# Optimization experiments

Hardware: AMD Instinct MI355X
Metric: run time of the kernel (lower is better)

## Reference

```python
import jax, jax.numpy as jnp
import numpy as np

NUM_CLASSES = 101
BATCH = 262144
LAMBDA = 1000.0


def setup_inputs() -> dict:
    key = jax.random.key(0)
    k1, k2 = jax.random.split(key)
    outputs = jax.random.normal(k1, (BATCH, NUM_CLASSES), dtype=jnp.float32)
    targets = jax.random.randint(k2, (BATCH,), 0, NUM_CLASSES, dtype=jnp.int64)
    return {"outputs": outputs, "targets": targets}


def reference(outputs, targets):
    B, C = outputs.shape
    targets = targets.reshape(-1)
    tf = targets.astype(outputs.dtype)

    probs = jax.nn.softmax(outputs, axis=1)                      # [B, C]
    labels = jnp.arange(C, dtype=outputs.dtype)                  # [C]
    pred_values = jnp.sum(probs * labels[None, :], axis=1)       # [B]
    centered = labels[None, :] - pred_values[:, None]            # [B, C]
    variance = jnp.sum(probs * centered * centered, axis=1)      # [B]
    variance = jnp.clip(variance, 1e-6, None)
    est_err = (pred_values - tf) ** 2
    concentrated_loss = jnp.mean(0.5 * jnp.log(variance) + est_err / (2.0 * variance))

    # Unimodal ordinal penalty, vectorized over the original double loop:
    # sign_j = -1 if j < target else +1; penalty = relu(-(p_j - p_{j+1}) * sign_j)
    j = jnp.arange(C - 1)                                        # [C-1]
    sign = jnp.where(j[None, :] < targets[:, None], -1.0, 1.0).astype(outputs.dtype)
    prob_diff = probs[:, :-1] - probs[:, 1:]                     # [B, C-1]
    penalty = jax.nn.relu(-prob_diff * sign)
    unimodal_loss = jnp.sum(penalty) / B
    weighted_unimodal_loss = LAMBDA * unimodal_loss

    total_loss = concentrated_loss + weighted_unimodal_loss
    return (total_loss, concentrated_loss, weighted_unimodal_loss)
```

## Files before the change

kernel.cpp:

```cpp
#include <hip/hip_runtime.h>


#define NT 128
#define TR 128
#define NC 101
#define TILE_F4 3232
#define PAD_F4 3328
#define NBLK 512
#define LAMBDA_W 1000.0

__device__ __forceinline__ void gload_lds16(const float4* g, float4* l)
{
    __builtin_amdgcn_global_load_lds(
        (const __attribute__((address_space(1))) void*)g,
        (__attribute__((address_space(3))) void*)l,
        16, 0, 0);
}

__device__ __forceinline__ void prefetch_tile(const float4* __restrict__ g4,
                                              float4* l4, int tid)
{
#pragma unroll
    for (int k = 0; k < 25; ++k)
        gload_lds16(g4 + k * NT + tid, l4 + k * NT + tid);
    if (tid < 32)
        gload_lds16(g4 + 25 * NT + tid, l4 + 25 * NT + tid);
}

__global__ __launch_bounds__(NT)
void ucl_row_kernel(const float* __restrict__ x,
                    const int* __restrict__ tgt,
                    float2* __restrict__ partial,
                    int ntiles)
{
    __shared__ __align__(16) float4 buf[2][PAD_F4];
    __shared__ float red[4];

    const int tid = threadIdx.x;
    const int bid = blockIdx.x;
    const int nb  = gridDim.x;

    const int tpb   = ntiles / nb;
    const int rem   = ntiles - tpb * nb;
    const int start = bid * tpb + (bid < rem ? bid : rem);
    const int cnt   = tpb + (bid < rem ? 1 : 0);

    const float4* __restrict__ x4 = (const float4*)x;

    int t_cur = tgt[(size_t)start * TR + tid];
    prefetch_tile(x4 + (size_t)start * TILE_F4, buf[0], tid);

    float conc = 0.f, pens = 0.f;

    for (int i = 0; i < cnt; ++i) {
        __syncthreads();

        if (i + 1 < cnt)
            prefetch_tile(x4 + (size_t)(start + i + 1) * TILE_F4,
                          buf[(i + 1) & 1], tid);
        int t_next = (i + 1 < cnt) ? tgt[(size_t)(start + i + 1) * TR + tid] : 0;

        const float* __restrict__ xr = (const float*)buf[i & 1] + tid * NC;
        const int t = t_cur;

        float e = __expf(xr[0]);
        float S = e, W = 0.f, Q = 0.f, pen = 0.f, ep = e;
#pragma unroll
        for (int j = 1; j < NC; ++j) {
            float e2 = __expf(xr[j]);
            float fj = (float)j;
            S += e2;
            W = fmaf(e2, fj, W);
            Q = fmaf(e2, fj * fj, Q);
            float d = ep - e2;
            float r = ((j - 1) < t) ? d : -d;
            pen += fmaxf(r, 0.f);
            ep = e2;
        }
        float pred = W / S;
        float var  = fmaxf(fmaf(-pred, pred, Q / S), 1e-6f);
        float err  = pred - (float)t;
        conc += 0.5f * __logf(var) + err * err / (2.0f * var);
        pens += pen / S;

        t_cur = t_next;
    }

#pragma unroll
    for (int off = 32; off > 0; off >>= 1) {
        conc += __shfl_down(conc, off);
        pens += __shfl_down(pens, off);
    }
    if ((tid & 63) == 0) {
        red[(tid >> 6) * 2 + 0] = conc;
        red[(tid >> 6) * 2 + 1] = pens;
    }
    __syncthreads();
    if (tid == 0)
        partial[bid] = make_float2(red[0] + red[2], red[1] + red[3]);
}

__global__ __launch_bounds__(256)
void ucl_finalize(const float2* __restrict__ partial,
                  float* __restrict__ out,
                  int nblocks, double invB)
{
    const int tid = threadIdx.x;
    double c = 0.0, p = 0.0;
    for (int i = tid; i < nblocks; i += 256) {
        float2 v = partial[i];
        c += (double)v.x;
        p += (double)v.y;
    }
#pragma unroll
    for (int off = 32; off > 0; off >>= 1) {
        c += __shfl_down(c, off);
        p += __shfl_down(p, off);
    }
    __shared__ double s[8];
    if ((tid & 63) == 0) { s[(tid >> 6) * 2] = c; s[(tid >> 6) * 2 + 1] = p; }
    __syncthreads();
    if (tid == 0) {
        double C = (s[0] + s[2] + s[4] + s[6]) * invB;
        double P = (s[1] + s[3] + s[5] + s[7]) * invB * LAMBDA_W;
        out[0] = (float)(C + P);
        out[1] = (float)C;
        out[2] = (float)P;
    }
}

extern "C" void kernel_launch(void* const* d_in, const int* in_sizes, int n_in,
                              void* d_out, int out_size, void* d_ws, size_t ws_size,
                              hipStream_t stream)
{
    const float* x   = (const float*)d_in[0];
    const int*   tgt = (const int*)d_in[1];
    float* out = (float*)d_out;
    float2* partial = (float2*)d_ws;

    const int B = in_sizes[1];
    const int ntiles = B / TR;
    const int blocks = (ntiles < NBLK) ? ntiles : NBLK;

    hipLaunchKernelGGL(ucl_row_kernel, dim3(blocks), dim3(NT), 0, stream,
                       x, tgt, partial, ntiles);
    hipLaunchKernelGGL(ucl_finalize, dim3(1), dim3(256), 0, stream,
                       partial, out, blocks, 1.0 / (double)B);
}
```

Measured before the change: 173.9 us.

## Split each row across four threads and launch one block per tile

Replaces the persistent double-buffered 512-block kernel with one 512-thread block per 128-row tile. Each row's 101 classes are split into four quarter scans, with one thread per quarter, and the partial sums are combined through LDS. The unimodal penalty is rewritten algebraically as a sum of positive diffs plus a boundary term minus the target probability. The aim is more waves in flight and a shorter serial exp chain per thread. In exchange it drops the cross-tile prefetch overlap and adds extra barriers and a per-block partial, with 2048 partials for the finalize to reduce.

```diff
diff --git a/kernel.cpp b/kernel.cpp
--- a/kernel.cpp
+++ b/kernel.cpp
@@ -1,12 +1,10 @@
 #include <hip/hip_runtime.h>
 
 
-#define NT 128
+#define NT 512
 #define TR 128
 #define NC 101
 #define TILE_F4 3232
-#define PAD_F4 3328
-#define NBLK 512
 #define LAMBDA_W 1000.0
 
 __device__ __forceinline__ void gload_lds16(const float4* g, float4* l)
@@ -17,73 +15,88 @@
         16, 0, 0);
 }
 
-__device__ __forceinline__ void prefetch_tile(const float4* __restrict__ g4,
-                                              float4* l4, int tid)
+template<int LO, int HI>
+__device__ __forceinline__ void scan_quarter(const float* __restrict__ xr, int t,
+                                             float& S, float& W, float& Q, float& pen)
 {
+    float e = __expf(xr[LO]);
+    S = e;
+    W = (float)LO * e;
+    Q = (float)(LO * LO) * e;
+    pen = 0.f;
+    float ep = e;
 #pragma unroll
-    for (int k = 0; k < 25; ++k)
-        gload_lds16(g4 + k * NT + tid, l4 + k * NT + tid);
-    if (tid < 32)
-        gload_lds16(g4 + 25 * NT + tid, l4 + 25 * NT + tid);
+    for (int j = LO + 1; j < HI; ++j) {
+        float e2 = __expf(xr[j]);
+        S += e2;
+        W = fmaf(e2, (float)j, W);
+        Q = fmaf(e2, (float)(j * j), Q);
+        pen += fmaxf(ep - e2, 0.f);
+        ep = e2;
+    }
+    if (HI < NC) {
+        float e2 = __expf(xr[HI]);
+        pen += fmaxf(ep - e2, 0.f);
+    } else {
+        pen += ep;
+    }
+    if (t >= LO && t < HI)
+        pen -= __expf(xr[t]);
 }
 
-__global__ __launch_bounds__(NT)
+__global__ __launch_bounds__(NT, 6)
 void ucl_row_kernel(const float* __restrict__ x,
                     const int* __restrict__ tgt,
-                    float2* __restrict__ partial,
-                    int ntiles)
+                    float2* __restrict__ partial)
 {
-    __shared__ __align__(16) float4 buf[2][PAD_F4];
+    __shared__ __align__(16) float tile[TR * NC];
     __shared__ float red[4];
 
     const int tid = threadIdx.x;
     const int bid = blockIdx.x;
-    const int nb  = gridDim.x;
+    const int r   = tid & (TR - 1);
+    const int q   = tid >> 7;
 
-    const int tpb   = ntiles / nb;
-    const int rem   = ntiles - tpb * nb;
-    const int start = bid * tpb + (bid < rem ? bid : rem);
-    const int cnt   = tpb + (bid < rem ? 1 : 0);
+    {
+        const float4* __restrict__ g4 =
+            (const float4*)(x + (size_t)bid * (TR * NC));
+        float4* l4 = (float4*)tile;
+#pragma unroll
+        for (int k = 0; k < 6; ++k)
+            gload_lds16(g4 + k * NT + tid, l4 + k * NT + tid);
+        if (tid < TILE_F4 - 6 * NT)
+            gload_lds16(g4 + 6 * NT + tid, l4 + 6 * NT + tid);
+    }
+    const int t = tgt[(size_t)bid * TR + r];
+    __syncthreads();
 
-    const float4* __restrict__ x4 = (const float4*)x;
+    const float* __restrict__ xr = tile + r * NC;
+    float S, W, Q, pen;
+    if      (q == 0) scan_quarter< 0,  26>(xr, t, S, W, Q, pen);
+    else if (q == 1) scan_quarter<26,  51>(xr, t, S, W, Q, pen);
+    else if (q == 2) scan_quarter<51,  76>(xr, t, S, W, Q, pen);
+    else             scan_quarter<76, 101>(xr, t, S, W, Q, pen);
 
-    int t_cur = tgt[(size_t)start * TR + tid];
-    prefetch_tile(x4 + (size_t)start * TILE_F4, buf[0], tid);
+    __syncthreads();
+    {
+        float4* p4 = (float4*)(tile + r * 20 + q * 4);
+        *p4 = make_float4(S, W, Q, pen);
+    }
+    __syncthreads();
 
     float conc = 0.f, pens = 0.f;
-
-    for (int i = 0; i < cnt; ++i) {
-        __syncthreads();
-
-        if (i + 1 < cnt)
-            prefetch_tile(x4 + (size_t)(start + i + 1) * TILE_F4,
-                          buf[(i + 1) & 1], tid);
-        int t_next = (i + 1 < cnt) ? tgt[(size_t)(start + i + 1) * TR + tid] : 0;
-
-        const float* __restrict__ xr = (const float*)buf[i & 1] + tid * NC;
-        const int t = t_cur;
-
-        float e = __expf(xr[0]);
-        float S = e, W = 0.f, Q = 0.f, pen = 0.f, ep = e;
-#pragma unroll
-        for (int j = 1; j < NC; ++j) {
-            float e2 = __expf(xr[j]);
-            float fj = (float)j;
-            S += e2;
-            W = fmaf(e2, fj, W);
-            Q = fmaf(e2, fj * fj, Q);
-            float d = ep - e2;
-            float r = ((j - 1) < t) ? d : -d;
-            pen += fmaxf(r, 0.f);
-            ep = e2;
-        }
-        float pred = W / S;
-        float var  = fmaxf(fmaf(-pred, pred, Q / S), 1e-6f);
+    if (q == 0) {
+        const float4* p4 = (const float4*)(tile + r * 20);
+        float4 a = p4[0], b = p4[1], c = p4[2], d = p4[3];
+        float Sf = a.x + b.x + c.x + d.x;
+        float Wf = a.y + b.y + c.y + d.y;
+        float Qf = a.z + b.z + c.z + d.z;
+        float Pf = a.w + b.w + c.w + d.w;
+        float pred = Wf / Sf;
+        float var  = fmaxf(fmaf(-pred, pred, Qf / Sf), 1e-6f);
         float err  = pred - (float)t;
-        conc += 0.5f * __logf(var) + err * err / (2.0f * var);
-        pens += pen / S;
-
-        t_cur = t_next;
+        conc = 0.5f * __logf(var) + err * err / (2.0f * var);
+        pens = Pf / Sf;
     }
 
 #pragma unroll
@@ -91,7 +104,7 @@
         conc += __shfl_down(conc, off);
         pens += __shfl_down(pens, off);
     }
-    if ((tid & 63) == 0) {
+    if (tid < 2 * TR && (tid & 63) == 0) {
         red[(tid >> 6) * 2 + 0] = conc;
         red[(tid >> 6) * 2 + 1] = pens;
     }
@@ -139,11 +152,10 @@
     float2* partial = (float2*)d_ws;
 
     const int B = in_sizes[1];
-    const int ntiles = B / TR;
-    const int blocks = (ntiles < NBLK) ? ntiles : NBLK;
+    const int blocks = B / TR;
 
     hipLaunchKernelGGL(ucl_row_kernel, dim3(blocks), dim3(NT), 0, stream,
-                       x, tgt, partial, ntiles);
+                       x, tgt, partial);
     hipLaunchKernelGGL(ucl_finalize, dim3(1), dim3(256), 0, stream,
                        partial, out, blocks, 1.0 / (double)B);
 }
```

Measured after the change: 154.8 us. -11.0%, faster.

## Process each row with 16 lanes and direct global loads instead of LDS tiles

Applied to the files above, without the earlier changes.

Replaces the one-thread-per-row design, which staged 128-row tiles in LDS through async global-to-LDS loads, with a layout where 16 lanes share a row and read it straight from global memory. Lane sums are combined with cross-lane shuffles. The unimodal penalty is rewritten algebraically as a sum of positive forward differences minus the target probability. Grid and block sizes change to 1024 blocks of 256 threads. This is meant to expose more parallelism and drop the LDS double buffering, at the cost of partly coalesced unaligned row loads and extra shuffles per row.

```diff
diff --git a/kernel.cpp b/kernel.cpp
--- a/kernel.cpp
+++ b/kernel.cpp
@@ -1,103 +1,94 @@
 #include <hip/hip_runtime.h>
 
 
-#define NT 128
-#define TR 128
 #define NC 101
-#define TILE_F4 3232
-#define PAD_F4 3328
-#define NBLK 512
 #define LAMBDA_W 1000.0
 
-__device__ __forceinline__ void gload_lds16(const float4* g, float4* l)
+__global__ __launch_bounds__(256)
+void ucl_stream_kernel(const float* __restrict__ x,
+                       const int* __restrict__ tgt,
+                       float2* __restrict__ partial,
+                       int ngroups)
 {
-    __builtin_amdgcn_global_load_lds(
-        (const __attribute__((address_space(1))) void*)g,
-        (__attribute__((address_space(3))) void*)l,
-        16, 0, 0);
-}
-
-__device__ __forceinline__ void prefetch_tile(const float4* __restrict__ g4,
-                                              float4* l4, int tid)
-{
-#pragma unroll
-    for (int k = 0; k < 25; ++k)
-        gload_lds16(g4 + k * NT + tid, l4 + k * NT + tid);
-    if (tid < 32)
-        gload_lds16(g4 + 25 * NT + tid, l4 + 25 * NT + tid);
-}
-
-__global__ __launch_bounds__(NT)
-void ucl_row_kernel(const float* __restrict__ x,
-                    const int* __restrict__ tgt,
-                    float2* __restrict__ partial,
-                    int ntiles)
-{
-    __shared__ __align__(16) float4 buf[2][PAD_F4];
-    __shared__ float red[4];
-
-    const int tid = threadIdx.x;
-    const int bid = blockIdx.x;
-    const int nb  = gridDim.x;
-
-    const int tpb   = ntiles / nb;
-    const int rem   = ntiles - tpb * nb;
-    const int start = bid * tpb + (bid < rem ? bid : rem);
-    const int cnt   = tpb + (bid < rem ? 1 : 0);
-
-    const float4* __restrict__ x4 = (const float4*)x;
-
-    int t_cur = tgt[(size_t)start * TR + tid];
-    prefetch_tile(x4 + (size_t)start * TILE_F4, buf[0], tid);
+    const int tid  = threadIdx.x;
+    const int lane = tid & 63;
+    const int s    = lane & 15;
+    const int gwave  = blockIdx.x * 4 + (tid >> 6);
+    const int nwaves = gridDim.x * 4;
 
     float conc = 0.f, pens = 0.f;
 
-    for (int i = 0; i < cnt; ++i) {
-        __syncthreads();
+    for (int g = gwave; g < ngroups; g += nwaves) {
+        const int row = g * 4 + (lane >> 4);
+        const float* __restrict__ xr = x + (size_t)row * NC;
+        const int t = tgt[row];
 
-        if (i + 1 < cnt)
-            prefetch_tile(x4 + (size_t)(start + i + 1) * TILE_F4,
-                          buf[(i + 1) & 1], tid);
-        int t_next = (i + 1 < cnt) ? tgt[(size_t)(start + i + 1) * TR + tid] : 0;
+        float e[7];
+#pragma unroll
+        for (int k = 0; k < 7; ++k) {
+            const int j = s + 16 * k;
+            e[k] = (j < NC) ? xr[j] : 0.f;
+        }
+#pragma unroll
+        for (int k = 0; k < 7; ++k) {
+            const int j = s + 16 * k;
+            float ee = __expf(e[k]);
+            e[k] = (j < NC) ? ee : 0.f;
+        }
 
-        const float* __restrict__ xr = (const float*)buf[i & 1] + tid * NC;
-        const int t = t_cur;
+        float S = 0.f, W = 0.f, Q = 0.f;
+#pragma unroll
+        for (int k = 0; k < 7; ++k) {
+            const float fj = (float)(s + 16 * k);
+            S += e[k];
+            W = fmaf(e[k], fj, W);
+            Q = fmaf(e[k], fj * fj, Q);
+        }
 
-        float e = __expf(xr[0]);
-        float S = e, W = 0.f, Q = 0.f, pen = 0.f, ep = e;
+        float pen = 0.f;
 #pragma unroll
-        for (int j = 1; j < NC; ++j) {
-            float e2 = __expf(xr[j]);
-            float fj = (float)j;
-            S += e2;
-            W = fmaf(e2, fj, W);
-            Q = fmaf(e2, fj * fj, Q);
-            float d = ep - e2;
-            float r = ((j - 1) < t) ? d : -d;
-            pen += fmaxf(r, 0.f);
-            ep = e2;
+        for (int k = 0; k < 7; ++k) {
+            float n1 = __shfl_down(e[k], 1);
+            float nx = (k < 6) ? __shfl(e[k + 1], lane & 48)
+                               : 0.f;
+            float en = (s == 15) ? nx : n1;
+            float d  = e[k] - en;
+            pen += fmaxf(d, 0.f);
+            const int j = s + 16 * k;
+            pen -= (j == t) ? e[k] : 0.f;
         }
-        float pred = W / S;
-        float var  = fmaxf(fmaf(-pred, pred, Q / S), 1e-6f);
-        float err  = pred - (float)t;
-        conc += 0.5f * __logf(var) + err * err / (2.0f * var);
-        pens += pen / S;
 
-        t_cur = t_next;
+#pragma unroll
+        for (int off = 1; off < 16; off <<= 1) {
+            S   += __shfl_xor(S, off);
+            W   += __shfl_xor(W, off);
+            Q   += __shfl_xor(Q, off);
+            pen += __shfl_xor(pen, off);
+        }
+
+        if (s == 0) {
+            float pred = W / S;
+            float var  = fmaxf(fmaf(-pred, pred, Q / S), 1e-6f);
+            float err  = pred - (float)t;
+            conc += 0.5f * __logf(var) + err * err / (2.0f * var);
+            pens += pen / S;
+        }
     }
 
-#pragma unroll
-    for (int off = 32; off > 0; off >>= 1) {
-        conc += __shfl_down(conc, off);
-        pens += __shfl_down(pens, off);
-    }
-    if ((tid & 63) == 0) {
+    conc += __shfl_down(conc, 16);
+    pens += __shfl_down(pens, 16);
+    conc += __shfl_down(conc, 32);
+    pens += __shfl_down(pens, 32);
+
+    __shared__ float red[8];
+    if (lane == 0) {
         red[(tid >> 6) * 2 + 0] = conc;
         red[(tid >> 6) * 2 + 1] = pens;
     }
     __syncthreads();
     if (tid == 0)
-        partial[bid] = make_float2(red[0] + red[2], red[1] + red[3]);
+        partial[blockIdx.x] = make_float2(red[0] + red[2] + red[4] + red[6],
+                                          red[1] + red[3] + red[5] + red[7]);
 }
 
 __global__ __launch_bounds__(256)
@@ -117,12 +108,12 @@
         c += __shfl_down(c, off);
         p += __shfl_down(p, off);
     }
-    __shared__ double s[8];
-    if ((tid & 63) == 0) { s[(tid >> 6) * 2] = c; s[(tid >> 6) * 2 + 1] = p; }
+    __shared__ double sm[8];
+    if ((tid & 63) == 0) { sm[(tid >> 6) * 2] = c; sm[(tid >> 6) * 2 + 1] = p; }
     __syncthreads();
     if (tid == 0) {
-        double C = (s[0] + s[2] + s[4] + s[6]) * invB;
-        double P = (s[1] + s[3] + s[5] + s[7]) * invB * LAMBDA_W;
+        double C = (sm[0] + sm[2] + sm[4] + sm[6]) * invB;
+        double P = (sm[1] + sm[3] + sm[5] + sm[7]) * invB * LAMBDA_W;
         out[0] = (float)(C + P);
         out[1] = (float)C;
         out[2] = (float)P;
@@ -139,11 +130,11 @@
     float2* partial = (float2*)d_ws;
 
     const int B = in_sizes[1];
-    const int ntiles = B / TR;
-    const int blocks = (ntiles < NBLK) ? ntiles : NBLK;
+    const int ngroups = B / 4;
+    const int blocks = 1024;
 
-    hipLaunchKernelGGL(ucl_row_kernel, dim3(blocks), dim3(NT), 0, stream,
-                       x, tgt, partial, ntiles);
+    hipLaunchKernelGGL(ucl_stream_kernel, dim3(blocks), dim3(256), 0, stream,
+                       x, tgt, partial, ngroups);
     hipLaunchKernelGGL(ucl_finalize, dim3(1), dim3(256), 0, stream,
                        partial, out, blocks, 1.0 / (double)B);
 }
```

After: 154.6 us, median of 2. 11.1% less time.
